# Performance work log

Measured on AMD Instinct MI355X. Metric: run time of the kernel, lower is better.

## Reference

```python
import jax, jax.numpy as jnp
import numpy as np

N_HEADS = 16


def sparsemax(z):
    """Sparsemax along the last axis (Martins & Astudillo 2016)."""
    S = z.shape[-1]
    z_sorted = -jnp.sort(-z, axis=-1)                      # descending
    cs = jnp.cumsum(z_sorted, axis=-1)
    k = jnp.arange(1, S + 1, dtype=z.dtype)
    support = (1.0 + k * z_sorted) > cs                    # bool mask of support
    k_z = jnp.sum(support.astype(jnp.int32), axis=-1, keepdims=True)  # support size >=1
    cs_k = jnp.take_along_axis(cs, k_z - 1, axis=-1)
    tau = (cs_k - 1.0) / k_z.astype(z.dtype)
    return jnp.maximum(z - tau, 0.0)


def setup_inputs() -> dict:
    key = jax.random.key(0)
    ks = jax.random.split(key, 5)
    B, S, D = 4, 1024, 1024
    scale = 1.0 / np.sqrt(D).astype(np.float32)
    return {
        "x": jax.random.normal(ks[0], (B, S, D), jnp.float32),
        "Wq": jax.random.normal(ks[1], (D, D), jnp.float32) * scale,
        "bq": jnp.zeros((D,), jnp.float32),
        "Wk": jax.random.normal(ks[2], (D, D), jnp.float32) * scale,
        "bk": jnp.zeros((D,), jnp.float32),
        "Wv": jax.random.normal(ks[3], (D, D), jnp.float32) * scale,
        "bv": jnp.zeros((D,), jnp.float32),
        "Wo": jax.random.normal(ks[4], (D, D), jnp.float32) * scale,
        "bo": jnp.zeros((D,), jnp.float32),
    }


def reference(x, Wq, bq, Wk, bk, Wv, bv, Wo, bo):
    B, S, D = x.shape
    H = N_HEADS
    dh = D // H
    q = x @ Wq + bq                                        # (B,S,D)
    k = x @ Wk + bk
    v = x @ Wv + bv
    # split to heads: (B,H,S,dh)
    qh = q.reshape(B, S, H, dh).transpose(0, 2, 1, 3)
    kh = k.reshape(B, S, H, dh).transpose(0, 2, 1, 3)
    logits = jnp.einsum("bhqd,bhkd->bhqk", qh, kh) / np.sqrt(dh).astype(np.float32)
    probs = sparsemax(logits)                              # (B,H,S,S)
    # shared V: mean over head components, replicated per head
    v_shared = v.reshape(B, S, H, dh).mean(axis=2)         # (B,S,dh)
    out_h = jnp.einsum("bhqk,bkd->bhqd", probs, v_shared)  # (B,H,S,dh)
    x_out = out_h.transpose(0, 2, 1, 3).reshape(B, S, D) @ Wo + bo
    avg_attention = probs.mean(axis=1)                     # (B,S,S)
    return (x_out, avg_attention)
```

## Files before the change

kernel.cpp:

```cpp
#include <hip/hip_runtime.h>

#define B_  4
#define S_  1024
#define D_  1024
#define H_  16
#define DH  64
#define BS  4096

typedef __bf16 bf16x8 __attribute__((ext_vector_type(8)));
typedef float  f32x4  __attribute__((ext_vector_type(4)));

__device__ __forceinline__ unsigned short f2bf(float f) {
    __bf16 b = (__bf16)f;
    return __builtin_bit_cast(unsigned short, b);
}
__device__ __forceinline__ float bf2f(unsigned short u) {
    return (float)__builtin_bit_cast(__bf16, u);
}
__device__ __forceinline__ void glds16(const void* g, void* l) {
    __builtin_amdgcn_global_load_lds((const __attribute__((address_space(1))) void*)g,
                                     (__attribute__((address_space(3))) void*)l, 16, 0, 0);
}

__global__ __launch_bounds__(256) void prep2(const float* __restrict__ Wq,
                                             const float* __restrict__ Wk,
                                             const float* __restrict__ Wo,
                                             const float* __restrict__ Wv,
                                             const float* __restrict__ bv,
                                             unsigned short* __restrict__ WqTh,
                                             unsigned short* __restrict__ WqTl,
                                             unsigned short* __restrict__ WkTh,
                                             unsigned short* __restrict__ WkTl,
                                             unsigned short* __restrict__ WoTh,
                                             unsigned short* __restrict__ WvTh,
                                             unsigned short* __restrict__ WvTl,
                                             float* __restrict__ bvp) {
    __shared__ float tile[32][33];
    int bid = blockIdx.x, tid = threadIdx.x;
    if (bid < 3072) {
        const float* W;
        unsigned short *Th, *Tl;
        int wantLo;
        if (bid < 1024)      { W = Wq; Th = WqTh; Tl = WqTl; wantLo = 1; }
        else if (bid < 2048) { W = Wk; Th = WkTh; Tl = WkTl; wantLo = 1; bid -= 1024; }
        else                 { W = Wo; Th = WoTh; Tl = nullptr; wantLo = 0; bid -= 2048; }
        int tn = bid & 31, tk = bid >> 5;
        int r = tid >> 3, c4 = (tid & 7) * 4;
        float4 v = *(const float4*)(W + (size_t)(tk * 32 + r) * D_ + tn * 32 + c4);
        tile[r][c4 + 0] = v.x;
        tile[r][c4 + 1] = v.y;
        tile[r][c4 + 2] = v.z;
        tile[r][c4 + 3] = v.w;
        __syncthreads();
        unsigned short hh[4], ll[4];
#pragma unroll
        for (int i = 0; i < 4; i++) {
            float f = tile[c4 + i][r];
            hh[i] = f2bf(f);
            ll[i] = f2bf(f - bf2f(hh[i]));
        }
        size_t off = (size_t)(tn * 32 + r) * D_ + tk * 32 + c4;
        *(uint2*)(Th + off) = make_uint2((unsigned)hh[0] | ((unsigned)hh[1] << 16),
                                         (unsigned)hh[2] | ((unsigned)hh[3] << 16));
        if (wantLo)
            *(uint2*)(Tl + off) = make_uint2((unsigned)ll[0] | ((unsigned)ll[1] << 16),
                                             (unsigned)ll[2] | ((unsigned)ll[3] << 16));
    } else if (bid < 3328) {
        int e = (bid - 3072) * 256 + tid;
        int d = e >> 6, j = e & 63;
        float s = 0.f;
#pragma unroll
        for (int hh = 0; hh < H_; hh++) s += Wv[(size_t)d * D_ + hh * DH + j];
        s *= (1.f / 16.f);
        unsigned short hi = f2bf(s);
        WvTh[(size_t)j * D_ + d] = hi;
        WvTl[(size_t)j * D_ + d] = f2bf(s - bf2f(hi));
        if (bid == 3072 && tid < 128) {
            float sb = 0.f;
            if (tid < 64) {
#pragma unroll
                for (int hh = 0; hh < H_; hh++) sb += bv[hh * DH + tid];
                sb *= (1.f / 16.f);
            }
            bvp[tid] = sb;
        }
    } else {
        int e = (bid - 3328) * 256 + tid;
        int row = 64 + (e >> 10), col = e & 1023;
        WvTh[(size_t)row * D_ + col] = 0;
        WvTl[(size_t)row * D_ + col] = 0;
    }
}

__global__ __launch_bounds__(256) void projg(const float* __restrict__ x,
                                             const unsigned short* __restrict__ WqTh, const unsigned short* __restrict__ WqTl,
                                             const unsigned short* __restrict__ WkTh, const unsigned short* __restrict__ WkTl,
                                             const unsigned short* __restrict__ WvTh, const unsigned short* __restrict__ WvTl,
                                             const float* __restrict__ bq, const float* __restrict__ bk,
                                             const float* __restrict__ bvp,
                                             unsigned short* __restrict__ qh, unsigned short* __restrict__ ql,
                                             unsigned short* __restrict__ kh, unsigned short* __restrict__ kl,
                                             float* __restrict__ vshb) {
    __shared__ unsigned short AhS[128 * 32];
    __shared__ unsigned short AlS[128 * 32];
    __shared__ unsigned short BhS[128 * 32];
    __shared__ unsigned short BlS[128 * 32];

    int tid = threadIdx.x, w = tid >> 6, lane = tid & 63;
    int m16 = lane & 15, qd = lane >> 4;
    int bn = blockIdx.x, bm = blockIdx.y;

    const unsigned short *Bh, *Bl;
    const float* bias;
    int mode;
    if (bn < 8)       { Bh = WqTh + (size_t)bn * 128 * D_;       Bl = WqTl + (size_t)bn * 128 * D_;       bias = bq + bn * 128;       mode = 0; }
    else if (bn < 16) { Bh = WkTh + (size_t)(bn - 8) * 128 * D_; Bl = WkTl + (size_t)(bn - 8) * 128 * D_; bias = bk + (bn - 8) * 128; mode = 1; }
    else              { Bh = WvTh; Bl = WvTl; bias = bvp; mode = 2; }

    int l4 = lane >> 2, c8 = (lane & 3) * 8;
    int rh = (w >> 1) * 64, chh = (w & 1) * 64;

    f32x4 acc[4][4];
#pragma unroll
    for (int it = 0; it < 4; it++)
#pragma unroll
        for (int jt = 0; jt < 4; jt++) acc[it][jt] = (f32x4){0.f, 0.f, 0.f, 0.f};

    int ra = tid >> 1, ca = (tid & 1) * 16;

    for (int k0 = 0; k0 < D_; k0 += 32) {
        const float* ax = x + (size_t)(bm * 128 + ra) * D_ + k0 + ca;
        float4 f0 = *(const float4*)(ax + 0);
        float4 f1 = *(const float4*)(ax + 4);
        float4 f2 = *(const float4*)(ax + 8);
        float4 f3 = *(const float4*)(ax + 12);
        __syncthreads();
        {
            float vv[16] = {f0.x, f0.y, f0.z, f0.w, f1.x, f1.y, f1.z, f1.w,
                            f2.x, f2.y, f2.z, f2.w, f3.x, f3.y, f3.z, f3.w};
            unsigned int hw[8], lw[8];
#pragma unroll
            for (int i = 0; i < 8; i++) {
                unsigned short h0 = f2bf(vv[2 * i]), h1 = f2bf(vv[2 * i + 1]);
                unsigned short l0 = f2bf(vv[2 * i] - bf2f(h0));
                unsigned short l1 = f2bf(vv[2 * i + 1] - bf2f(h1));
                hw[i] = (unsigned)h0 | ((unsigned)h1 << 16);
                lw[i] = (unsigned)l0 | ((unsigned)l1 << 16);
            }
            char* ah = (char*)AhS + ra * 64 + ca * 2;
            char* al = (char*)AlS + ra * 64 + ca * 2;
            *(uint4*)(ah + 0)  = make_uint4(hw[0], hw[1], hw[2], hw[3]);
            *(uint4*)(ah + 16) = make_uint4(hw[4], hw[5], hw[6], hw[7]);
            *(uint4*)(al + 0)  = make_uint4(lw[0], lw[1], lw[2], lw[3]);
            *(uint4*)(al + 16) = make_uint4(lw[4], lw[5], lw[6], lw[7]);
        }
        {
            const unsigned short* gbh = Bh + (size_t)(w * 32 + l4) * D_ + k0 + c8;
            const unsigned short* gbl = Bl + (size_t)(w * 32 + l4) * D_ + k0 + c8;
            glds16(gbh,                     (char*)BhS + w * 2048);
            glds16(gbh + (size_t)16 * D_,   (char*)BhS + w * 2048 + 1024);
            glds16(gbl,                     (char*)BlS + w * 2048);
            glds16(gbl + (size_t)16 * D_,   (char*)BlS + w * 2048 + 1024);
        }
        __syncthreads();
        bf16x8 ah[4], al[4], bh[4], bl[4];
#pragma unroll
        for (int it = 0; it < 4; it++) {
            ah[it] = *(const bf16x8*)((char*)AhS + (rh + it * 16 + m16) * 64 + qd * 16);
            al[it] = *(const bf16x8*)((char*)AlS + (rh + it * 16 + m16) * 64 + qd * 16);
        }
#pragma unroll
        for (int jt = 0; jt < 4; jt++) {
            bh[jt] = *(const bf16x8*)((char*)BhS + (chh + jt * 16 + m16) * 64 + qd * 16);
            bl[jt] = *(const bf16x8*)((char*)BlS + (chh + jt * 16 + m16) * 64 + qd * 16);
        }
#pragma unroll
        for (int it = 0; it < 4; it++)
#pragma unroll
            for (int jt = 0; jt < 4; jt++) {
                acc[it][jt] = __builtin_amdgcn_mfma_f32_16x16x32_bf16(ah[it], bh[jt], acc[it][jt], 0, 0, 0);
                acc[it][jt] = __builtin_amdgcn_mfma_f32_16x16x32_bf16(ah[it], bl[jt], acc[it][jt], 0, 0, 0);
                acc[it][jt] = __builtin_amdgcn_mfma_f32_16x16x32_bf16(al[it], bh[jt], acc[it][jt], 0, 0, 0);
            }
    }
#pragma unroll
    for (int it = 0; it < 4; it++)
#pragma unroll
        for (int jt = 0; jt < 4; jt++)
#pragma unroll
            for (int r = 0; r < 4; r++) {
                int R = bm * 128 + rh + it * 16 + qd * 4 + r;
                int c = chh + jt * 16 + m16;
                float v = acc[it][jt][r] + bias[c];
                if (mode == 0) {
                    v *= 0.125f;
                    unsigned short h0 = f2bf(v);
                    qh[(size_t)R * D_ + bn * 128 + c] = h0;
                    ql[(size_t)R * D_ + bn * 128 + c] = f2bf(v - bf2f(h0));
                } else if (mode == 1) {
                    unsigned short h0 = f2bf(v);
                    kh[(size_t)R * D_ + (bn - 8) * 128 + c] = h0;
                    kl[(size_t)R * D_ + (bn - 8) * 128 + c] = f2bf(v - bf2f(h0));
                } else {
                    if (c < 64) vshb[(size_t)R * 64 + c] = v;
                }
            }
}

__global__ __launch_bounds__(256) void outg(const unsigned short* __restrict__ A,
                                            const unsigned short* __restrict__ Bh,
                                            const float* __restrict__ bias,
                                            float* __restrict__ C) {
    __shared__ unsigned short AhS[64 * 32];
    __shared__ unsigned short BhS[64 * 32];

    int tid = threadIdx.x, w = tid >> 6, lane = tid & 63;
    int m16 = lane & 15, qd = lane >> 4;
    int bn = blockIdx.x, bm = blockIdx.y;
    int l4 = lane >> 2, c8 = (lane & 3) * 8;
    int rh = (w >> 1) * 32, chh = (w & 1) * 32;

    f32x4 acc[2][2];
#pragma unroll
    for (int it = 0; it < 2; it++)
#pragma unroll
        for (int jt = 0; jt < 2; jt++) acc[it][jt] = (f32x4){0.f, 0.f, 0.f, 0.f};

    for (int k0 = 0; k0 < D_; k0 += 32) {
        __syncthreads();
        {
            const unsigned short* ga = A + (size_t)(bm * 64 + w * 16 + l4) * D_ + k0 + c8;
            glds16(ga, (char*)AhS + w * 1024);
            const unsigned short* gb = Bh + (size_t)(bn * 64 + w * 16 + l4) * D_ + k0 + c8;
            glds16(gb, (char*)BhS + w * 1024);
        }
        __syncthreads();
        bf16x8 ah[2], bh[2];
#pragma unroll
        for (int it = 0; it < 2; it++)
            ah[it] = *(const bf16x8*)((char*)AhS + (rh + it * 16 + m16) * 64 + qd * 16);
#pragma unroll
        for (int jt = 0; jt < 2; jt++)
            bh[jt] = *(const bf16x8*)((char*)BhS + (chh + jt * 16 + m16) * 64 + qd * 16);
#pragma unroll
        for (int it = 0; it < 2; it++)
#pragma unroll
            for (int jt = 0; jt < 2; jt++)
                acc[it][jt] = __builtin_amdgcn_mfma_f32_16x16x32_bf16(ah[it], bh[jt], acc[it][jt], 0, 0, 0);
    }
#pragma unroll
    for (int it = 0; it < 2; it++)
#pragma unroll
        for (int jt = 0; jt < 2; jt++)
#pragma unroll
            for (int r = 0; r < 4; r++) {
                int R = bm * 64 + rh + it * 16 + qd * 4 + r;
                int cc = bn * 64 + chh + jt * 16 + m16;
                C[(size_t)R * D_ + cc] = acc[it][jt][r] + bias[cc];
            }
}

#define CCAP 48
__global__ __launch_bounds__(256, 4) void attn8(const unsigned short* __restrict__ qh,
                                                const unsigned short* __restrict__ ql,
                                                const unsigned short* __restrict__ kh,
                                                const unsigned short* __restrict__ kl,
                                                const float* __restrict__ vsh,
                                                unsigned short* __restrict__ och,
                                                unsigned short* __restrict__ sidx,
                                                unsigned short* __restrict__ sval,
                                                int* __restrict__ scnt) {
    __shared__ __align__(16) char KST[32768];
    __shared__ float smM[4][16];
    __shared__ float smS[4][16], smC[4][16];
    __shared__ float tau0s[16];
    __shared__ float taus[16];
    __shared__ int   ccnt[16];
    __shared__ int   ovfAny;
    __shared__ int   scnt16[16];

    float (*candV)[CCAP] = (float (*)[CCAP])(KST);
    short (*candI)[CCAP] = (short (*)[CCAP])(KST + 3072);
    float (*slotV)[16]   = (float (*)[16])(KST + 4608);
    short (*slotI)[16]   = (short (*)[16])(KST + 5632);

    int tid = threadIdx.x, w = tid >> 6, lane = tid & 63;
    int m16 = lane & 15, qd = lane >> 4;

    int bid = blockIdx.x;
    int xcd = bid & 7;
    int j   = bid >> 3;
    int bh  = ((j >> 6) << 3) | xcd;
    int qt  = j & 63;
    int bb  = bh >> 4, h = bh & 15;
    int row0g = bb * S_ + qt * 16;
    int kbase = bb * S_;

    bf16x8 aH[2], aL[2];
#pragma unroll
    for (int c = 0; c < 2; c++) {
        size_t off = (size_t)(row0g + m16) * D_ + h * DH + c * 32 + qd * 8;
        aH[c] = *(const bf16x8*)(qh + off);
        aL[c] = *(const bf16x8*)(ql + off);
    }

    f32x4 Cfr[16];
#pragma unroll
    for (int t = 0; t < 16; t++) Cfr[t] = (f32x4){0.f, 0.f, 0.f, 0.f};

    char* myK = KST + w * 8192;
    {
        int sr = lane >> 3;
        int sc = (lane & 7) ^ sr;
        const unsigned short* ksh = kh + (size_t)(kbase + w * 256 + sr) * D_ + h * DH + sc * 8;
        const unsigned short* ksl = kl + (size_t)(kbase + w * 256 + sr) * D_ + h * DH + sc * 8;

#define STAGE_K(t, buf) do {                                        \
        size_t o_ = (size_t)(t) * 16 * D_;                          \
        char* db_ = myK + (buf) * 4096;                             \
        glds16(ksh + o_,                  db_);                     \
        glds16(ksh + o_ + (size_t)8 * D_, db_ + 1024);              \
        glds16(ksl + o_,                  db_ + 2048);              \
        glds16(ksl + o_ + (size_t)8 * D_, db_ + 3072);              \
    } while (0)

        int sw0 = m16 * 128 + (((qd    ) ^ (m16 & 7)) << 4);
        int sw1 = m16 * 128 + (((4 + qd) ^ (m16 & 7)) << 4);

        STAGE_K(0, 0);
        asm volatile("s_waitcnt vmcnt(0)" ::: "memory");
        __builtin_amdgcn_sched_barrier(0);

#pragma unroll
        for (int t = 0; t < 16; t++) {
            if (t < 15) {
                STAGE_K(t + 1, (t + 1) & 1);
                asm volatile("s_waitcnt vmcnt(4)" ::: "memory");
            } else {
                asm volatile("s_waitcnt vmcnt(0)" ::: "memory");
            }
            __builtin_amdgcn_sched_barrier(0);
            const char* tbuf = myK + (t & 1) * 4096;
            bf16x8 bfh0 = *(const bf16x8*)(tbuf + sw0);
            bf16x8 bfh1 = *(const bf16x8*)(tbuf + sw1);
            bf16x8 bfl0 = *(const bf16x8*)(tbuf + 2048 + sw0);
            bf16x8 bfl1 = *(const bf16x8*)(tbuf + 2048 + sw1);
            f32x4 a = Cfr[t];
            __builtin_amdgcn_s_setprio(1);
            a = __builtin_amdgcn_mfma_f32_16x16x32_bf16(aH[0], bfh0, a, 0, 0, 0);
            a = __builtin_amdgcn_mfma_f32_16x16x32_bf16(aH[1], bfh1, a, 0, 0, 0);
            a = __builtin_amdgcn_mfma_f32_16x16x32_bf16(aH[0], bfl0, a, 0, 0, 0);
            a = __builtin_amdgcn_mfma_f32_16x16x32_bf16(aH[1], bfl1, a, 0, 0, 0);
            a = __builtin_amdgcn_mfma_f32_16x16x32_bf16(aL[0], bfh0, a, 0, 0, 0);
            a = __builtin_amdgcn_mfma_f32_16x16x32_bf16(aL[1], bfh1, a, 0, 0, 0);
            __builtin_amdgcn_s_setprio(0);
            Cfr[t] = a;
        }
#undef STAGE_K
    }

    float mxr[4];
#pragma unroll
    for (int r = 0; r < 4; r++) mxr[r] = -3.0e38f;
#pragma unroll
    for (int t = 0; t < 16; t++)
#pragma unroll
        for (int r = 0; r < 4; r++) mxr[r] = fmaxf(mxr[r], Cfr[t][r]);
#pragma unroll
    for (int off = 8; off >= 1; off >>= 1)
#pragma unroll
        for (int r = 0; r < 4; r++) mxr[r] = fmaxf(mxr[r], __shfl_xor(mxr[r], off, 16));
    if (m16 == 0)
#pragma unroll
        for (int r = 0; r < 4; r++) smM[w][qd * 4 + r] = mxr[r];
    if (tid < 16) ccnt[tid] = 0;
    if (tid == 0) ovfAny = 0;
    __syncthreads();
    if (tid < 16)
        tau0s[tid] = fmaxf(fmaxf(smM[0][tid], smM[1][tid]), fmaxf(smM[2][tid], smM[3][tid])) - 1.0f;
    __syncthreads();

    float t0r[4];
#pragma unroll
    for (int r = 0; r < 4; r++) t0r[r] = tau0s[qd * 4 + r];

#pragma unroll
    for (int t = 0; t < 16; t++)
#pragma unroll
        for (int r = 0; r < 4; r++) {
            float z = Cfr[t][r];
            int row = qd * 4 + r;
            if (z > t0r[r]) {
                int pos = atomicAdd(&ccnt[row], 1);
                if (pos < CCAP) {
                    candV[row][pos] = z;
                    candI[row][pos] = (short)(w * 256 + t * 16 + m16);
                }
            }
        }
    __syncthreads();
    if (tid < 16 && ccnt[tid] > CCAP) ovfAny = 1;

    int prow = tid >> 4, pc = tid & 15;
    int nc = ccnt[prow];
    float tau = tau0s[prow];
    float z0 = -3.0e38f, z1 = -3.0e38f, z2 = -3.0e38f;
    if (nc <= CCAP) {
        z0 = (pc < nc)      ? candV[prow][pc]      : -3.0e38f;
        z1 = (pc + 16 < nc) ? candV[prow][pc + 16] : -3.0e38f;
        z2 = (pc + 32 < nc) ? candV[prow][pc + 32] : -3.0e38f;
        for (int it = 0; it < CCAP; it++) {
            float s = 0.f, c = 0.f;
            if (z0 > tau) { s += z0; c += 1.f; }
            if (z1 > tau) { s += z1; c += 1.f; }
            if (z2 > tau) { s += z2; c += 1.f; }
#pragma unroll
            for (int off = 8; off >= 1; off >>= 1) {
                s += __shfl_xor(s, off, 16);
                c += __shfl_xor(c, off, 16);
            }
            float tnew = (s - 1.f) / c;
            if (tnew > tau) tau = tnew; else break;
        }
    }
    if (pc == 0) taus[prow] = tau;
    if (tid < 16) scnt16[tid] = 0;
    __syncthreads();

    if (!ovfAny) {
        if (z0 > tau) {
            int sl = atomicAdd(&scnt16[prow], 1);
            if (sl < 16) { slotI[prow][sl] = candI[prow][pc]; slotV[prow][sl] = z0 - tau; }
        }
        if (z1 > tau) {
            int sl = atomicAdd(&scnt16[prow], 1);
            if (sl < 16) { slotI[prow][sl] = candI[prow][pc + 16]; slotV[prow][sl] = z1 - tau; }
        }
        if (z2 > tau) {
            int sl = atomicAdd(&scnt16[prow], 1);
            if (sl < 16) { slotI[prow][sl] = candI[prow][pc + 32]; slotV[prow][sl] = z2 - tau; }
        }
        __syncthreads();
    } else {
        for (int it = 0; it < 64; it++) {
            float s[4], c[4];
#pragma unroll
            for (int r = 0; r < 4; r++) { s[r] = 0.f; c[r] = 0.f; }
#pragma unroll
            for (int t = 0; t < 16; t++)
#pragma unroll
                for (int r = 0; r < 4; r++) {
                    float z = Cfr[t][r];
                    if (z > taus[qd * 4 + r]) { s[r] += z; c[r] += 1.f; }
                }
#pragma unroll
            for (int off = 8; off >= 1; off >>= 1)
#pragma unroll
                for (int r = 0; r < 4; r++) {
                    s[r] += __shfl_xor(s[r], off, 16);
                    c[r] += __shfl_xor(c[r], off, 16);
                }
            if (m16 == 0)
#pragma unroll
                for (int r = 0; r < 4; r++) {
                    smS[w][qd * 4 + r] = s[r];
                    smC[w][qd * 4 + r] = c[r];
                }
            __syncthreads();
            int done = 1;
            if (tid < 16) {
                float S = smS[0][tid] + smS[1][tid] + smS[2][tid] + smS[3][tid];
                float C = smC[0][tid] + smC[1][tid] + smC[2][tid] + smC[3][tid];
                float tnew = (S - 1.f) / C;
                if (C > 0.f && tnew > taus[tid]) { taus[tid] = tnew; done = 0; }
            }
            if (__syncthreads_and(done)) break;
        }
#pragma unroll
        for (int t = 0; t < 16; t++)
#pragma unroll
            for (int r = 0; r < 4; r++) {
                int row = qd * 4 + r;
                float p = Cfr[t][r] - taus[row];
                if (p > 0.f) {
                    int sl = atomicAdd(&scnt16[row], 1);
                    if (sl < 16) {
                        slotI[row][sl] = (short)(w * 256 + t * 16 + m16);
                        slotV[row][sl] = p;
                    }
                }
            }
        __syncthreads();
    }

    int nsl = min(scnt16[prow], 16);
    f32x4 v0 = *(const f32x4*)&slotV[prow][0];
    f32x4 v1 = *(const f32x4*)&slotV[prow][4];
    f32x4 v2 = *(const f32x4*)&slotV[prow][8];
    f32x4 v3 = *(const f32x4*)&slotV[prow][12];
    const uint4* sIv = (const uint4*)&slotI[prow][0];
    uint4 i0 = sIv[0], i1 = sIv[1];
    float pA[16] = {v0[0], v0[1], v0[2], v0[3], v1[0], v1[1], v1[2], v1[3],
                    v2[0], v2[1], v2[2], v2[3], v3[0], v3[1], v3[2], v3[3]};
    unsigned wI[8] = {i0.x, i0.y, i0.z, i0.w, i1.x, i1.y, i1.z, i1.w};
    float4 accq = make_float4(0.f, 0.f, 0.f, 0.f);
#pragma unroll
    for (int sl = 0; sl < 16; sl++) {
        float p = (sl < nsl) ? pA[sl] : 0.f;
        int key = (int)((wI[sl >> 1] >> ((sl & 1) * 16)) & 1023u);
        float4 vv = *(const float4*)(vsh + (size_t)(kbase + key) * DH + pc * 4);
        accq.x += p * vv.x;
        accq.y += p * vv.y;
        accq.z += p * vv.z;
        accq.w += p * vv.w;
    }
    {
        unsigned short b0 = f2bf(accq.x), b1 = f2bf(accq.y), b2 = f2bf(accq.z), b3 = f2bf(accq.w);
        *(uint2*)(och + (size_t)(row0g + prow) * D_ + h * DH + pc * 4) =
            make_uint2((unsigned)b0 | ((unsigned)b1 << 16), (unsigned)b2 | ((unsigned)b3 << 16));
    }
    {
        size_t base = ((size_t)(row0g + prow) * H_ + h) * 16;
        if (pc == 0) scnt[(row0g + prow) * H_ + h] = nsl;
        if (pc < nsl) {
            sidx[base + pc] = (unsigned short)slotI[prow][pc];
            sval[base + pc] = f2bf(slotV[prow][pc]);
        }
    }
}

__global__ __launch_bounds__(256) void avg_reduce(const unsigned short* __restrict__ sidx,
                                                  const unsigned short* __restrict__ sval,
                                                  const int* __restrict__ scnt,
                                                  float* __restrict__ avg) {
    __shared__ float accv[1024];
    int tid = threadIdx.x;
    int grow = blockIdx.x;
    for (int i = tid; i < 1024; i += 256) accv[i] = 0.f;
    __syncthreads();
    int h = tid >> 4, sl = tid & 15;
    int n = scnt[grow * H_ + h];
    if (sl < n) {
        size_t base = ((size_t)grow * H_ + h) * 16;
        int idx = sidx[base + sl];
        float v = bf2f(sval[base + sl]);
        atomicAdd(&accv[idx], v);
    }
    __syncthreads();
    float* dst = avg + (size_t)grow * S_;
    for (int i = tid; i < 256; i += 256) {
        float4 o;
        o.x = accv[i * 4 + 0] * 0.0625f;
        o.y = accv[i * 4 + 1] * 0.0625f;
        o.z = accv[i * 4 + 2] * 0.0625f;
        o.w = accv[i * 4 + 3] * 0.0625f;
        *(float4*)(dst + i * 4) = o;
    }
}

extern "C" void kernel_launch(void* const* d_in, const int* in_sizes, int n_in,
                              void* d_out, int out_size, void* d_ws, size_t ws_size,
                              hipStream_t stream) {
    const float* x  = (const float*)d_in[0];
    const float* Wq = (const float*)d_in[1];
    const float* bq = (const float*)d_in[2];
    const float* Wk = (const float*)d_in[3];
    const float* bk = (const float*)d_in[4];
    const float* Wv = (const float*)d_in[5];
    const float* bv = (const float*)d_in[6];
    const float* Wo = (const float*)d_in[7];
    const float* bo = (const float*)d_in[8];

    float* xout = (float*)d_out;
    float* avg  = xout + (size_t)BS * D_;

    char* ws = (char*)d_ws;
    unsigned short* qhB  = (unsigned short*)(ws + 0);
    unsigned short* qlB  = (unsigned short*)(ws + (8u << 20));
    unsigned short* khB  = (unsigned short*)(ws + (16u << 20));
    unsigned short* klB  = (unsigned short*)(ws + (24u << 20));
    unsigned short* WqTh = (unsigned short*)(ws + (32u << 20));
    unsigned short* WqTl = (unsigned short*)(ws + (34u << 20));
    unsigned short* WkTh = (unsigned short*)(ws + (36u << 20));
    unsigned short* WkTl = (unsigned short*)(ws + (38u << 20));
    unsigned short* ochB = WqTh;
    unsigned short* WoTh = (unsigned short*)(ws + (40u << 20));
    unsigned short* WvTh = (unsigned short*)(ws + (42u << 20));
    unsigned short* WvTl = (unsigned short*)(ws + (42u << 20) + (256u << 10));
    float* bvp = (float*)(ws + (42u << 20) + (512u << 10));
    float* vshb = (float*)(ws + (43u << 20));
    unsigned short* sidx = (unsigned short*)(ws + (44u << 20));
    unsigned short* sval = (unsigned short*)(ws + (46u << 20));
    int* scnt = (int*)(ws + (48u << 20));

    prep2<<<3584, 256, 0, stream>>>(Wq, Wk, Wo, Wv, bv, WqTh, WqTl, WkTh, WkTl, WoTh, WvTh, WvTl, bvp);
    projg<<<dim3(17, 32), 256, 0, stream>>>(x, WqTh, WqTl, WkTh, WkTl, WvTh, WvTl,
                                            bq, bk, bvp, qhB, qlB, khB, klB, vshb);
    attn8<<<4096, 256, 0, stream>>>(qhB, qlB, khB, klB, vshb, ochB, sidx, sval, scnt);
    avg_reduce<<<4096, 256, 0, stream>>>(sidx, sval, scnt, avg);
    outg<<<dim3(16, 64), 256, 0, stream>>>(ochB, WoTh, bo, xout);
}
```

Baseline: 352.2 us.

## Recompute QK logits instead of holding them in registers to raise occupancy

Stops keeping the 16 logit tiles in registers across the sparsemax phases. Each pass that needs the logits (max, candidate gather, and the overflow fallback passes) now recomputes them from a single-buffered LDS K stage. This frees registers and halves the K staging LDS so launch bounds can go from 4 to 6 waves per SIMD. In exchange the QK MFMA work and K loads at least double, single buffering exposes load latency, and the overflow path recomputes logits on every iteration.

```diff
diff --git a/kernel.cpp b/kernel.cpp
--- a/kernel.cpp
+++ b/kernel.cpp
@@ -261,7 +261,7 @@
 }
 
 #define CCAP 48
-__global__ __launch_bounds__(256, 4) void attn8(const unsigned short* __restrict__ qh,
+__global__ __launch_bounds__(256, 6) void attn8(const unsigned short* __restrict__ qh,
                                                 const unsigned short* __restrict__ ql,
                                                 const unsigned short* __restrict__ kh,
                                                 const unsigned short* __restrict__ kl,
@@ -270,7 +270,9 @@
                                                 unsigned short* __restrict__ sidx,
                                                 unsigned short* __restrict__ sval,
                                                 int* __restrict__ scnt) {
-    __shared__ __align__(16) char KST[32768];
+    __shared__ __align__(16) char KST[16384];
+    __shared__ __align__(16) float candVS[16][CCAP];
+    __shared__ short candIS[16][CCAP];
     __shared__ float smM[4][16];
     __shared__ float smS[4][16], smC[4][16];
     __shared__ float tau0s[16];
@@ -279,10 +281,8 @@
     __shared__ int   ovfAny;
     __shared__ int   scnt16[16];
 
-    float (*candV)[CCAP] = (float (*)[CCAP])(KST);
-    short (*candI)[CCAP] = (short (*)[CCAP])(KST + 3072);
-    float (*slotV)[16]   = (float (*)[16])(KST + 4608);
-    short (*slotI)[16]   = (short (*)[16])(KST + 5632);
+    float (*slotV)[16] = (float (*)[16])((char*)candVS);
+    short (*slotI)[16] = (short (*)[16])((char*)candVS + 1024);
 
     int tid = threadIdx.x, w = tid >> 6, lane = tid & 63;
     int m16 = lane & 15, qd = lane >> 4;
@@ -304,68 +304,58 @@
         aL[c] = *(const bf16x8*)(ql + off);
     }
 
-    f32x4 Cfr[16];
-#pragma unroll
-    for (int t = 0; t < 16; t++) Cfr[t] = (f32x4){0.f, 0.f, 0.f, 0.f};
-
-    char* myK = KST + w * 8192;
-    {
-        int sr = lane >> 3;
-        int sc = (lane & 7) ^ sr;
-        const unsigned short* ksh = kh + (size_t)(kbase + w * 256 + sr) * D_ + h * DH + sc * 8;
-        const unsigned short* ksl = kl + (size_t)(kbase + w * 256 + sr) * D_ + h * DH + sc * 8;
-
-#define STAGE_K(t, buf) do {                                        \
-        size_t o_ = (size_t)(t) * 16 * D_;                          \
-        char* db_ = myK + (buf) * 4096;                             \
-        glds16(ksh + o_,                  db_);                     \
-        glds16(ksh + o_ + (size_t)8 * D_, db_ + 1024);              \
-        glds16(ksl + o_,                  db_ + 2048);              \
-        glds16(ksl + o_ + (size_t)8 * D_, db_ + 3072);              \
+    char* myK = KST + w * 4096;
+    int sr = lane >> 3;
+    int sc = (lane & 7) ^ sr;
+    const unsigned short* ksh = kh + (size_t)(kbase + w * 256 + sr) * D_ + h * DH + sc * 8;
+    const unsigned short* ksl = kl + (size_t)(kbase + w * 256 + sr) * D_ + h * DH + sc * 8;
+
+#define STAGE_K(t) do {                                         \
+        size_t o_ = (size_t)(t) * 16 * D_;                      \
+        glds16(ksh + o_,                  myK);                 \
+        glds16(ksh + o_ + (size_t)8 * D_, myK + 1024);          \
+        glds16(ksl + o_,                  myK + 2048);          \
+        glds16(ksl + o_ + (size_t)8 * D_, myK + 3072);          \
     } while (0)
 
-        int sw0 = m16 * 128 + (((qd    ) ^ (m16 & 7)) << 4);
-        int sw1 = m16 * 128 + (((4 + qd) ^ (m16 & 7)) << 4);
-
-        STAGE_K(0, 0);
-        asm volatile("s_waitcnt vmcnt(0)" ::: "memory");
-        __builtin_amdgcn_sched_barrier(0);
-
-#pragma unroll
-        for (int t = 0; t < 16; t++) {
-            if (t < 15) {
-                STAGE_K(t + 1, (t + 1) & 1);
-                asm volatile("s_waitcnt vmcnt(4)" ::: "memory");
-            } else {
-                asm volatile("s_waitcnt vmcnt(0)" ::: "memory");
-            }
-            __builtin_amdgcn_sched_barrier(0);
-            const char* tbuf = myK + (t & 1) * 4096;
-            bf16x8 bfh0 = *(const bf16x8*)(tbuf + sw0);
-            bf16x8 bfh1 = *(const bf16x8*)(tbuf + sw1);
-            bf16x8 bfl0 = *(const bf16x8*)(tbuf + 2048 + sw0);
-            bf16x8 bfl1 = *(const bf16x8*)(tbuf + 2048 + sw1);
-            f32x4 a = Cfr[t];
-            __builtin_amdgcn_s_setprio(1);
-            a = __builtin_amdgcn_mfma_f32_16x16x32_bf16(aH[0], bfh0, a, 0, 0, 0);
-            a = __builtin_amdgcn_mfma_f32_16x16x32_bf16(aH[1], bfh1, a, 0, 0, 0);
-            a = __builtin_amdgcn_mfma_f32_16x16x32_bf16(aH[0], bfl0, a, 0, 0, 0);
-            a = __builtin_amdgcn_mfma_f32_16x16x32_bf16(aH[1], bfl1, a, 0, 0, 0);
-            a = __builtin_amdgcn_mfma_f32_16x16x32_bf16(aL[0], bfh0, a, 0, 0, 0);
-            a = __builtin_amdgcn_mfma_f32_16x16x32_bf16(aL[1], bfh1, a, 0, 0, 0);
-            __builtin_amdgcn_s_setprio(0);
-            Cfr[t] = a;
-        }
-#undef STAGE_K
+    int sw0 = m16 * 128 + (((qd    ) ^ (m16 & 7)) << 4);
+    int sw1 = m16 * 128 + (((4 + qd) ^ (m16 & 7)) << 4);
+
+#define QK_TILE(t, STAGE_NEXT, NEXT_T, a)                                   \
+    {                                                                       \
+        asm volatile("s_waitcnt vmcnt(0)" ::: "memory");                    \
+        __builtin_amdgcn_sched_barrier(0);                                  \
+        bf16x8 bfh0 = *(const bf16x8*)(myK + sw0);                          \
+        bf16x8 bfh1 = *(const bf16x8*)(myK + sw1);                          \
+        bf16x8 bfl0 = *(const bf16x8*)(myK + 2048 + sw0);                   \
+        bf16x8 bfl1 = *(const bf16x8*)(myK + 2048 + sw1);                   \
+        asm volatile("s_waitcnt lgkmcnt(0)" ::: "memory");                  \
+        __builtin_amdgcn_sched_barrier(0);                                  \
+        if (STAGE_NEXT) STAGE_K(NEXT_T);                                    \
+        a = (f32x4){0.f, 0.f, 0.f, 0.f};                                    \
+        __builtin_amdgcn_s_setprio(1);                                      \
+        a = __builtin_amdgcn_mfma_f32_16x16x32_bf16(aH[0], bfh0, a, 0, 0, 0); \
+        a = __builtin_amdgcn_mfma_f32_16x16x32_bf16(aH[1], bfh1, a, 0, 0, 0); \
+        a = __builtin_amdgcn_mfma_f32_16x16x32_bf16(aH[0], bfl0, a, 0, 0, 0); \
+        a = __builtin_amdgcn_mfma_f32_16x16x32_bf16(aH[1], bfl1, a, 0, 0, 0); \
+        a = __builtin_amdgcn_mfma_f32_16x16x32_bf16(aL[0], bfh0, a, 0, 0, 0); \
+        a = __builtin_amdgcn_mfma_f32_16x16x32_bf16(aL[1], bfh1, a, 0, 0, 0); \
+        __builtin_amdgcn_s_setprio(0);                                      \
     }
 
     float mxr[4];
 #pragma unroll
     for (int r = 0; r < 4; r++) mxr[r] = -3.0e38f;
-#pragma unroll
-    for (int t = 0; t < 16; t++)
-#pragma unroll
-        for (int r = 0; r < 4; r++) mxr[r] = fmaxf(mxr[r], Cfr[t][r]);
+    STAGE_K(0);
+#pragma unroll
+    for (int t = 0; t < 16; t++) {
+        f32x4 a;
+        QK_TILE(t, t < 15, t + 1, a);
+#pragma unroll
+        for (int r = 0; r < 4; r++) mxr[r] = fmaxf(mxr[r], a[r]);
+    }
+    STAGE_K(0);
+
 #pragma unroll
     for (int off = 8; off >= 1; off >>= 1)
 #pragma unroll
@@ -385,19 +375,22 @@
     for (int r = 0; r < 4; r++) t0r[r] = tau0s[qd * 4 + r];
 
 #pragma unroll
-    for (int t = 0; t < 16; t++)
+    for (int t = 0; t < 16; t++) {
+        f32x4 a;
+        QK_TILE(t, t < 15, t + 1, a);
 #pragma unroll
         for (int r = 0; r < 4; r++) {
-            float z = Cfr[t][r];
+            float z = a[r];
             int row = qd * 4 + r;
             if (z > t0r[r]) {
                 int pos = atomicAdd(&ccnt[row], 1);
                 if (pos < CCAP) {
-                    candV[row][pos] = z;
-                    candI[row][pos] = (short)(w * 256 + t * 16 + m16);
+                    candVS[row][pos] = z;
+                    candIS[row][pos] = (short)(w * 256 + t * 16 + m16);
                 }
             }
         }
+    }
     __syncthreads();
     if (tid < 16 && ccnt[tid] > CCAP) ovfAny = 1;
 
@@ -405,10 +398,13 @@
     int nc = ccnt[prow];
     float tau = tau0s[prow];
     float z0 = -3.0e38f, z1 = -3.0e38f, z2 = -3.0e38f;
+    short i0r = candIS[prow][pc];
+    short i1r = candIS[prow][pc + 16];
+    short i2r = candIS[prow][pc + 32];
     if (nc <= CCAP) {
-        z0 = (pc < nc)      ? candV[prow][pc]      : -3.0e38f;
-        z1 = (pc + 16 < nc) ? candV[prow][pc + 16] : -3.0e38f;
-        z2 = (pc + 32 < nc) ? candV[prow][pc + 32] : -3.0e38f;
+        z0 = (pc < nc)      ? candVS[prow][pc]      : -3.0e38f;
+        z1 = (pc + 16 < nc) ? candVS[prow][pc + 16] : -3.0e38f;
+        z2 = (pc + 32 < nc) ? candVS[prow][pc + 32] : -3.0e38f;
         for (int it = 0; it < CCAP; it++) {
             float s = 0.f, c = 0.f;
             if (z0 > tau) { s += z0; c += 1.f; }
@@ -430,29 +426,33 @@
     if (!ovfAny) {
         if (z0 > tau) {
             int sl = atomicAdd(&scnt16[prow], 1);
-            if (sl < 16) { slotI[prow][sl] = candI[prow][pc]; slotV[prow][sl] = z0 - tau; }
+            if (sl < 16) { slotI[prow][sl] = i0r; slotV[prow][sl] = z0 - tau; }
         }
         if (z1 > tau) {
             int sl = atomicAdd(&scnt16[prow], 1);
-            if (sl < 16) { slotI[prow][sl] = candI[prow][pc + 16]; slotV[prow][sl] = z1 - tau; }
+            if (sl < 16) { slotI[prow][sl] = i1r; slotV[prow][sl] = z1 - tau; }
         }
         if (z2 > tau) {
             int sl = atomicAdd(&scnt16[prow], 1);
-            if (sl < 16) { slotI[prow][sl] = candI[prow][pc + 32]; slotV[prow][sl] = z2 - tau; }
+            if (sl < 16) { slotI[prow][sl] = i2r; slotV[prow][sl] = z2 - tau; }
         }
         __syncthreads();
     } else {
         for (int it = 0; it < 64; it++) {
-            float s[4], c[4];
-#pragma unroll
-            for (int r = 0; r < 4; r++) { s[r] = 0.f; c[r] = 0.f; }
-#pragma unroll
-            for (int t = 0; t < 16; t++)
+            float s[4], c[4], tsr[4];
+#pragma unroll
+            for (int r = 0; r < 4; r++) { s[r] = 0.f; c[r] = 0.f; tsr[r] = taus[qd * 4 + r]; }
+            STAGE_K(0);
+#pragma unroll
+            for (int t = 0; t < 16; t++) {
+                f32x4 a;
+                QK_TILE(t, t < 15, t + 1, a);
 #pragma unroll
                 for (int r = 0; r < 4; r++) {
-                    float z = Cfr[t][r];
-                    if (z > taus[qd * 4 + r]) { s[r] += z; c[r] += 1.f; }
+                    float z = a[r];
+                    if (z > tsr[r]) { s[r] += z; c[r] += 1.f; }
                 }
+            }
 #pragma unroll
             for (int off = 8; off >= 1; off >>= 1)
 #pragma unroll
@@ -476,12 +476,18 @@
             }
             if (__syncthreads_and(done)) break;
         }
-#pragma unroll
-        for (int t = 0; t < 16; t++)
+        float tfr[4];
+#pragma unroll
+        for (int r = 0; r < 4; r++) tfr[r] = taus[qd * 4 + r];
+        STAGE_K(0);
+#pragma unroll
+        for (int t = 0; t < 16; t++) {
+            f32x4 a;
+            QK_TILE(t, t < 15, t + 1, a);
 #pragma unroll
             for (int r = 0; r < 4; r++) {
                 int row = qd * 4 + r;
-                float p = Cfr[t][r] - taus[row];
+                float p = a[r] - tfr[r];
                 if (p > 0.f) {
                     int sl = atomicAdd(&scnt16[row], 1);
                     if (sl < 16) {
@@ -490,8 +496,11 @@
                     }
                 }
             }
+        }
         __syncthreads();
     }
+#undef QK_TILE
+#undef STAGE_K
 
     int nsl = min(scnt16[prow], 16);
     f32x4 v0 = *(const f32x4*)&slotV[prow][0];
```

Measured after the change: 892.5 us. 2.53x slower.

## Fuse head-averaged attention accumulation into attn kernel via global atomics

Applied to the files above, without the earlier changes.

Drops the separate avg_reduce kernel and the sidx/sval/scnt scratch buffers. Each attention thread now atomically adds its sparse probability, scaled by 1/16, straight into the avg output. The avg buffer is zeroed by extra blocks appended to the prep kernel. This saves one kernel launch and the scratch write and read round trip, at the cost of global atomics with possible contention across heads, plus 4096 extra zeroing blocks that write the full 16 MB avg matrix.

```diff
diff --git a/kernel.cpp b/kernel.cpp
--- a/kernel.cpp
+++ b/kernel.cpp
@@ -34,7 +34,8 @@
                                              unsigned short* __restrict__ WoTh,
                                              unsigned short* __restrict__ WvTh,
                                              unsigned short* __restrict__ WvTl,
-                                             float* __restrict__ bvp) {
+                                             float* __restrict__ bvp,
+                                             float* __restrict__ avg) {
     __shared__ float tile[32][33];
     int bid = blockIdx.x, tid = threadIdx.x;
     if (bid < 3072) {
@@ -84,11 +85,14 @@
             }
             bvp[tid] = sb;
         }
-    } else {
+    } else if (bid < 3584) {
         int e = (bid - 3328) * 256 + tid;
         int row = 64 + (e >> 10), col = e & 1023;
         WvTh[(size_t)row * D_ + col] = 0;
         WvTl[(size_t)row * D_ + col] = 0;
+    } else {
+        int e = (bid - 3584) * 256 + tid;
+        *(float4*)(avg + (size_t)e * 4) = make_float4(0.f, 0.f, 0.f, 0.f);
     }
 }
 
@@ -267,9 +271,7 @@
                                                 const unsigned short* __restrict__ kl,
                                                 const float* __restrict__ vsh,
                                                 unsigned short* __restrict__ och,
-                                                unsigned short* __restrict__ sidx,
-                                                unsigned short* __restrict__ sval,
-                                                int* __restrict__ scnt) {
+                                                float* __restrict__ avg) {
     __shared__ __align__(16) char KST[32768];
     __shared__ float smM[4][16];
     __shared__ float smS[4][16], smC[4][16];
@@ -519,42 +521,9 @@
         *(uint2*)(och + (size_t)(row0g + prow) * D_ + h * DH + pc * 4) =
             make_uint2((unsigned)b0 | ((unsigned)b1 << 16), (unsigned)b2 | ((unsigned)b3 << 16));
     }
-    {
-        size_t base = ((size_t)(row0g + prow) * H_ + h) * 16;
-        if (pc == 0) scnt[(row0g + prow) * H_ + h] = nsl;
-        if (pc < nsl) {
-            sidx[base + pc] = (unsigned short)slotI[prow][pc];
-            sval[base + pc] = f2bf(slotV[prow][pc]);
-        }
-    }
-}
-
-__global__ __launch_bounds__(256) void avg_reduce(const unsigned short* __restrict__ sidx,
-                                                  const unsigned short* __restrict__ sval,
-                                                  const int* __restrict__ scnt,
-                                                  float* __restrict__ avg) {
-    __shared__ float accv[1024];
-    int tid = threadIdx.x;
-    int grow = blockIdx.x;
-    for (int i = tid; i < 1024; i += 256) accv[i] = 0.f;
-    __syncthreads();
-    int h = tid >> 4, sl = tid & 15;
-    int n = scnt[grow * H_ + h];
-    if (sl < n) {
-        size_t base = ((size_t)grow * H_ + h) * 16;
-        int idx = sidx[base + sl];
-        float v = bf2f(sval[base + sl]);
-        atomicAdd(&accv[idx], v);
-    }
-    __syncthreads();
-    float* dst = avg + (size_t)grow * S_;
-    for (int i = tid; i < 256; i += 256) {
-        float4 o;
-        o.x = accv[i * 4 + 0] * 0.0625f;
-        o.y = accv[i * 4 + 1] * 0.0625f;
-        o.z = accv[i * 4 + 2] * 0.0625f;
-        o.w = accv[i * 4 + 3] * 0.0625f;
-        *(float4*)(dst + i * 4) = o;
+    if (pc < nsl) {
+        int key = (int)((wI[pc >> 1] >> ((pc & 1) * 16)) & 1023u);
+        atomicAdd(avg + (size_t)(row0g + prow) * S_ + key, pA[pc] * 0.0625f);
     }
 }
 
@@ -589,14 +558,10 @@
     unsigned short* WvTl = (unsigned short*)(ws + (42u << 20) + (256u << 10));
     float* bvp = (float*)(ws + (42u << 20) + (512u << 10));
     float* vshb = (float*)(ws + (43u << 20));
-    unsigned short* sidx = (unsigned short*)(ws + (44u << 20));
-    unsigned short* sval = (unsigned short*)(ws + (46u << 20));
-    int* scnt = (int*)(ws + (48u << 20));
-
-    prep2<<<3584, 256, 0, stream>>>(Wq, Wk, Wo, Wv, bv, WqTh, WqTl, WkTh, WkTl, WoTh, WvTh, WvTl, bvp);
+
+    prep2<<<7680, 256, 0, stream>>>(Wq, Wk, Wo, Wv, bv, WqTh, WqTl, WkTh, WkTl, WoTh, WvTh, WvTl, bvp, avg);
     projg<<<dim3(17, 32), 256, 0, stream>>>(x, WqTh, WqTl, WkTh, WkTl, WvTh, WvTl,
                                             bq, bk, bvp, qhB, qlB, khB, klB, vshb);
-    attn8<<<4096, 256, 0, stream>>>(qhB, qlB, khB, klB, vshb, ochB, sidx, sval, scnt);
-    avg_reduce<<<4096, 256, 0, stream>>>(sidx, sval, scnt, avg);
+    attn8<<<4096, 256, 0, stream>>>(qhB, qlB, khB, klB, vshb, ochB, avg);
     outg<<<dim3(16, 64), 256, 0, stream>>>(ochB, WoTh, bo, xout);
 }
```

Result: no change. 348.6 us (-1.0%).
